# Optimization experiments

Hardware: AMD Instinct MI355X
Metric: run time of the kernel (lower is better)

The kernel has to match this reference:

```python
import jax, jax.numpy as jnp
import numpy as np

N_HEAD = 16
N_KV_HEAD = 4
HEAD_DIM = 64  # n_embd // n_head = 1024 // 16
N_EMBD = 1024


def _alibi_bias(T, n_head, head_dim):
    # slopes: start = 2**(-2**(-(log2(H)-3))); slope_i = start**(i+1)
    start = 2.0 ** (-2.0 ** (-(np.log2(n_head) - 3.0)))
    slopes = jnp.asarray(start ** np.arange(1, n_head + 1), dtype=jnp.float32)  # [H]
    rel = (jnp.arange(T, dtype=jnp.float32)[None, :]
           - jnp.arange(T, dtype=jnp.float32)[:, None])  # [T,T], rel[i,j] = j - i
    bias = slopes[:, None, None] * rel[None, :, :]  # [H,T,T]
    # Faithful to the torch module: masked_fill(-inf) is then OVERWRITTEN by
    # torch.tril, which zeroes the upper triangle. Net effect: lower-tri alibi
    # values, 0 above the diagonal (NO causal masking).
    bias = jnp.tril(bias)
    return bias * (head_dim ** -0.5)  # extra scale applied in forward


def setup_inputs() -> dict:
    key = jax.random.key(0)
    ks = jax.random.split(key, 5)
    B, T, C = 4, 2048, N_EMBD
    w_scale = 0.02
    return {
        "x": jax.random.normal(ks[0], (B, T, C), dtype=jnp.float32),
        "Wq": jax.random.normal(ks[1], (C, C), dtype=jnp.float32) * w_scale,
        "Wkv": jax.random.normal(ks[2], (2 * N_KV_HEAD * HEAD_DIM, C), dtype=jnp.float32) * w_scale,
        "Wproj": jax.random.normal(ks[3], (C, C), dtype=jnp.float32) * w_scale,
        "bproj": jnp.zeros((C,), dtype=jnp.float32),
    }


def reference(x, Wq, Wkv, Wproj, bproj):
    B, T, C = x.shape
    H, KVH, D = N_HEAD, N_KV_HEAD, HEAD_DIM
    ratio = H // KVH

    q = jnp.einsum('btc,ec->bte', x, Wq).reshape(B, T, H, D).transpose(0, 2, 1, 3)  # [B,H,T,D]
    kv = jnp.einsum('btc,ec->bte', x, Wkv)  # [B,T,2*KVH*D]
    k, v = jnp.split(kv, 2, axis=-1)
    k = k.reshape(B, T, KVH, D).transpose(0, 2, 1, 3)  # [B,KVH,T,D]
    v = v.reshape(B, T, KVH, D).transpose(0, 2, 1, 3)
    # torch .repeat tiles whole blocks: query head h uses kv head h % KVH
    k = jnp.tile(k, (1, ratio, 1, 1))  # [B,H,T,D]
    v = jnp.tile(v, (1, ratio, 1, 1))

    bias = _alibi_bias(T, H, D)  # [H,T,T], already *= D**-0.5
    scores = jnp.einsum('bhtd,bhsd->bhts', q, k) * (D ** -0.5) + bias[None]
    attn = jax.nn.softmax(scores, axis=-1)
    out = jnp.einsum('bhts,bhsd->bhtd', attn, v)  # [B,H,T,D]
    out = out.transpose(0, 2, 1, 3).reshape(B, T, C)
    return jnp.einsum('btc,ec->bte', out, Wproj) + bproj
```

## Files before the change

kernel.cpp:

```cpp
#include <hip/hip_runtime.h>
#include <hip/hip_bf16.h>
#include <cstdint>

typedef __bf16 bf16;
typedef bf16 bf16x4 __attribute__((ext_vector_type(4)));
typedef bf16 bf16x8 __attribute__((ext_vector_type(8)));
typedef float f32x4 __attribute__((ext_vector_type(4)));

#define MFMA16(a, b, c) __builtin_amdgcn_mfma_f32_16x16x32_bf16((a), (b), (c), 0, 0, 0)

__device__ inline void async16(const bf16* g, bf16* l) {
  __builtin_amdgcn_global_load_lds(
      (const __attribute__((address_space(1))) void*)g,
      (__attribute__((address_space(3))) void*)l, 16, 0, 0);
}

__device__ inline void lds_barrier() {
  asm volatile("s_waitcnt lgkmcnt(0)\n\ts_barrier" ::: "memory");
}

__global__ void cast_f32_to_bf16(const float* __restrict__ src,
                                 bf16* __restrict__ dst, int n4) {
  int i = blockIdx.x * blockDim.x + threadIdx.x;
  if (i < n4) {
    const float4 v = ((const float4*)src)[i];
    bf16x4 o;
    o.x = (bf16)v.x; o.y = (bf16)v.y; o.z = (bf16)v.z; o.w = (bf16)v.w;
    ((bf16x4*)dst)[i] = o;
  }
}

__global__ __launch_bounds__(256, 2)
void gemm_qkv(const bf16* __restrict__ A, const bf16* __restrict__ B,
              bf16* __restrict__ qb, bf16* __restrict__ kb, bf16* __restrict__ vb) {
  constexpr int K = 1024;
  __shared__ bf16 sA[128 * 64];
  __shared__ bf16 sB[128 * 64];
  const int tid = threadIdx.x;
  const int lane = tid & 63, wid = tid >> 6;
  const int col = lane & 15, quad = lane >> 4;
  const int wm = wid >> 1, wn = wid & 1;
  const int m0 = blockIdx.y * 128, n0 = blockIdx.x * 128;
  const int c7 = col & 7;

  f32x4 acc[4][4];
  const f32x4 z = {0.f, 0.f, 0.f, 0.f};
#pragma unroll
  for (int mi = 0; mi < 4; mi++)
#pragma unroll
    for (int ni = 0; ni < 4; ni++) acc[mi][ni] = z;

  for (int k0 = 0; k0 < K; k0 += 64) {
    __syncthreads();
#pragma unroll
    for (int c = 0; c < 4; ++c) {
      const int idx = c * 256 + tid;
      const int row = idx >> 3, kc = idx & 7;
      const int gkc = kc ^ (row & 7);
      async16(&A[(size_t)(m0 + row) * K + k0 + gkc * 8], &sA[idx * 8]);
      async16(&B[(size_t)(n0 + row) * K + k0 + gkc * 8], &sB[idx * 8]);
    }
    __syncthreads();
#pragma unroll
    for (int ks = 0; ks < 2; ++ks) {
      bf16x8 af[4], bfr[4];
#pragma unroll
      for (int i = 0; i < 4; i++)
        af[i] = *(const bf16x8*)&sA[(wm * 64 + i * 16 + col) * 64 +
                                    (((ks * 4 + quad) ^ c7) << 3)];
#pragma unroll
      for (int i = 0; i < 4; i++)
        bfr[i] = *(const bf16x8*)&sB[(wn * 64 + i * 16 + col) * 64 +
                                     (((ks * 4 + quad) ^ c7) << 3)];
#pragma unroll
      for (int mi = 0; mi < 4; mi++)
#pragma unroll
        for (int ni = 0; ni < 4; ni++)
          acc[mi][ni] = MFMA16(af[mi], bfr[ni], acc[mi][ni]);
    }
  }
#pragma unroll
  for (int mi = 0; mi < 4; mi++) {
#pragma unroll
    for (int ni = 0; ni < 4; ni++) {
      const int e = n0 + wn * 64 + ni * 16 + col;
#pragma unroll
      for (int r = 0; r < 4; r++) {
        const int m = m0 + wm * 64 + mi * 16 + quad * 4 + r;
        const int bb = m >> 11, t = m & 2047;
        const bf16 val = (bf16)acc[mi][ni][r];
        if (e < 1024) {
          qb[(((size_t)bb * 16 + (e >> 6)) * 2048 + t) * 64 + (e & 63)] = val;
        } else if (e < 1280) {
          const int f = e - 1024;
          kb[(((size_t)bb * 4 + (f >> 6)) * 2048 + t) * 64 + (f & 63)] = val;
        } else {
          const int f = e - 1280;
          vb[(((size_t)bb * 4 + (f >> 6)) * 2048 + t) * 64 + (f & 63)] = val;
        }
      }
    }
  }
}

__global__ __launch_bounds__(256, 2)
void gemm_proj(const bf16* __restrict__ A, const bf16* __restrict__ B,
               const float* __restrict__ bias, float* __restrict__ out) {
  constexpr int K = 1024;
  __shared__ bf16 sA[128 * 64];
  __shared__ bf16 sB[128 * 64];
  const int tid = threadIdx.x;
  const int lane = tid & 63, wid = tid >> 6;
  const int col = lane & 15, quad = lane >> 4;
  const int wm = wid >> 1, wn = wid & 1;
  const int m0 = blockIdx.y * 128, n0 = blockIdx.x * 128;
  const int c7 = col & 7;

  f32x4 acc[4][4];
  const f32x4 z = {0.f, 0.f, 0.f, 0.f};
#pragma unroll
  for (int mi = 0; mi < 4; mi++)
#pragma unroll
    for (int ni = 0; ni < 4; ni++) acc[mi][ni] = z;

  for (int k0 = 0; k0 < K; k0 += 64) {
    __syncthreads();
#pragma unroll
    for (int c = 0; c < 4; ++c) {
      const int idx = c * 256 + tid;
      const int row = idx >> 3, kc = idx & 7;
      const int gkc = kc ^ (row & 7);
      async16(&A[(size_t)(m0 + row) * K + k0 + gkc * 8], &sA[idx * 8]);
      async16(&B[(size_t)(n0 + row) * K + k0 + gkc * 8], &sB[idx * 8]);
    }
    __syncthreads();
#pragma unroll
    for (int ks = 0; ks < 2; ++ks) {
      bf16x8 af[4], bfr[4];
#pragma unroll
      for (int i = 0; i < 4; i++)
        af[i] = *(const bf16x8*)&sA[(wm * 64 + i * 16 + col) * 64 +
                                    (((ks * 4 + quad) ^ c7) << 3)];
#pragma unroll
      for (int i = 0; i < 4; i++)
        bfr[i] = *(const bf16x8*)&sB[(wn * 64 + i * 16 + col) * 64 +
                                     (((ks * 4 + quad) ^ c7) << 3)];
#pragma unroll
      for (int mi = 0; mi < 4; mi++)
#pragma unroll
        for (int ni = 0; ni < 4; ni++)
          acc[mi][ni] = MFMA16(af[mi], bfr[ni], acc[mi][ni]);
    }
  }
#pragma unroll
  for (int mi = 0; mi < 4; mi++) {
#pragma unroll
    for (int ni = 0; ni < 4; ni++) {
      const int e = n0 + wn * 64 + ni * 16 + col;
      const float be = bias[e];
#pragma unroll
      for (int r = 0; r < 4; r++) {
        const int m = m0 + wm * 64 + mi * 16 + quad * 4 + r;
        out[(size_t)m * 1024 + e] = acc[mi][ni][r] + be;
      }
    }
  }
}

__global__ __launch_bounds__(256, 2)
void attn_alibi(const bf16* __restrict__ qb, const bf16* __restrict__ kb,
                const bf16* __restrict__ vb, bf16* __restrict__ ob) {
  __shared__ bf16 sK[64 * 72];
  __shared__ bf16 sVt[64 * 72];
  __shared__ bf16 sPt[4][64 * 72];
  __shared__ float sL[4][64];
  const int tid = threadIdx.x;
  const int lane = tid & 63, wid = tid >> 6;
  const int col = lane & 15, quad = lane >> 4;
  const int bh = blockIdx.y;
  const int b = bh >> 4, h = bh & 15, kvh = h & 3;
  const int qbase = __builtin_amdgcn_readfirstlane(blockIdx.x * 256 + wid * 64);

  const bf16* qptr = qb + ((size_t)(b * 16 + h) * 2048 + qbase) * 64;
  const bf16* kptr = kb + ((size_t)(b * 4 + kvh) * 2048) * 64;
  const bf16* vptr = vb + ((size_t)(b * 4 + kvh) * 2048) * 64;

  bf16x8 bq[4][2];
#pragma unroll
  for (int ni = 0; ni < 4; ni++)
#pragma unroll
    for (int ks = 0; ks < 2; ks++)
      bq[ni][ks] = *(const bf16x8*)&qptr[(ni * 16 + col) * 64 + ks * 32 + quad * 8];

  f32x4 O[4][4];
  const f32x4 z = {0.f, 0.f, 0.f, 0.f};
#pragma unroll
  for (int mi = 0; mi < 4; mi++)
#pragma unroll
    for (int nd = 0; nd < 4; nd++) O[mi][nd] = z;
  float lsum[4] = {0.f, 0.f, 0.f, 0.f};

  const float c1 = 0.125f * 1.44269504f;
  const float cb = exp2f(-0.5f * (float)(h + 1)) * c1;
  const int qoff = quad * 4 - col;

  const int r0 = tid >> 3, r1 = 32 + (tid >> 3), kc = tid & 7;

  bf16x8 kr0, kr1, vr0, vr1;
  kr0 = *(const bf16x8*)&kptr[(size_t)r0 * 64 + kc * 8];
  kr1 = *(const bf16x8*)&kptr[(size_t)r1 * 64 + kc * 8];
  vr0 = *(const bf16x8*)&vptr[(size_t)r0 * 64 + kc * 8];
  vr1 = *(const bf16x8*)&vptr[(size_t)r1 * 64 + kc * 8];

  for (int c0 = 0; c0 < 2048; c0 += 64) {
    lds_barrier();
    *(bf16x8*)&sK[r0 * 72 + kc * 8] = kr0;
    *(bf16x8*)&sK[r1 * 72 + kc * 8] = kr1;
    {
      const int blk0 = r0 >> 3, rl0 = r0 & 7;
      const int blk1 = r1 >> 3, rl1 = r1 & 7;
#pragma unroll
      for (int j = 0; j < 8; j++) {
        sVt[(kc * 8 + j) * 72 + ((blk0 ^ kc) << 3) + rl0] = vr0[j];
        sVt[(kc * 8 + j) * 72 + ((blk1 ^ kc) << 3) + rl1] = vr1[j];
      }
    }
    {
      const int cn = (c0 + 64 < 2048) ? c0 + 64 : 0;
      kr0 = *(const bf16x8*)&kptr[(size_t)(cn + r0) * 64 + kc * 8];
      kr1 = *(const bf16x8*)&kptr[(size_t)(cn + r1) * 64 + kc * 8];
      vr0 = *(const bf16x8*)&vptr[(size_t)(cn + r0) * 64 + kc * 8];
      vr1 = *(const bf16x8*)&vptr[(size_t)(cn + r1) * 64 + kc * 8];
    }
    lds_barrier();

    f32x4 S[4][4];
#pragma unroll
    for (int mi = 0; mi < 4; mi++)
#pragma unroll
      for (int ni = 0; ni < 4; ni++) S[mi][ni] = z;
#pragma unroll
    for (int ks = 0; ks < 2; ks++) {
      bf16x8 ak[4];
#pragma unroll
      for (int mi = 0; mi < 4; mi++)
        ak[mi] = *(const bf16x8*)&sK[(mi * 16 + col) * 72 + ks * 32 + quad * 8];
#pragma unroll
      for (int mi = 0; mi < 4; mi++)
#pragma unroll
        for (int ni = 0; ni < 4; ni++)
          S[mi][ni] = MFMA16(ak[mi], bq[ni][ks], S[mi][ni]);
    }

    bf16* sp = sPt[wid];
#pragma unroll
    for (int ni = 0; ni < 4; ni++) {
      f32x4 p[4];
#pragma unroll
      for (int mi = 0; mi < 4; mi++) {
        const int U = c0 + mi * 16 - qbase - ni * 16;
        if (U <= -15) {
          const float bb = cb * (float)(U + qoff);
#pragma unroll
          for (int r = 0; r < 4; r++)
            p[mi][r] = __builtin_amdgcn_exp2f(S[mi][ni][r] * c1 + (bb + cb * (float)r));
        } else if (U >= 16) {
#pragma unroll
          for (int r = 0; r < 4; r++)
            p[mi][r] = __builtin_amdgcn_exp2f(S[mi][ni][r] * c1);
        } else {
          const float relf = (float)(U + qoff);
#pragma unroll
          for (int r = 0; r < 4; r++) {
            const float rr = relf + (float)r;
            const float bb = (rr <= 0.f) ? cb * rr : 0.f;
            p[mi][r] = __builtin_amdgcn_exp2f(S[mi][ni][r] * c1 + bb);
          }
        }
      }
      f32x4 t = (p[0] + p[1]) + (p[2] + p[3]);
      lsum[ni] += (t.x + t.y) + (t.z + t.w);
#pragma unroll
      for (int mi = 0; mi < 4; mi++) {
        bf16x4 w;
#pragma unroll
        for (int r = 0; r < 4; r++) w[r] = (bf16)p[mi][r];
        *(bf16x4*)&sp[(ni * 16 + col) * 72 + mi * 16 + quad * 4] = w;
      }
    }

#pragma unroll
    for (int ks = 0; ks < 2; ks++) {
      bf16x8 ap[4], bv[4];
#pragma unroll
      for (int mi = 0; mi < 4; mi++)
        ap[mi] = *(const bf16x8*)&sp[(mi * 16 + col) * 72 + ks * 32 + quad * 8];
#pragma unroll
      for (int nd = 0; nd < 4; nd++) {
        const int d = nd * 16 + col;
        bv[nd] = *(const bf16x8*)&sVt[d * 72 + (((ks * 4 + quad) ^ (d >> 3)) << 3)];
      }
#pragma unroll
      for (int mi = 0; mi < 4; mi++)
#pragma unroll
        for (int nd = 0; nd < 4; nd++)
          O[mi][nd] = MFMA16(ap[mi], bv[nd], O[mi][nd]);
    }
  }

#pragma unroll
  for (int ni = 0; ni < 4; ni++) {
    float l = lsum[ni];
    l += __shfl_xor(l, 16);
    l += __shfl_xor(l, 32);
    lsum[ni] = l;
  }
  __syncthreads();
  if (quad == 0) {
#pragma unroll
    for (int ni = 0; ni < 4; ni++) sL[wid][ni * 16 + col] = lsum[ni];
  }
  __syncthreads();

#pragma unroll
  for (int mi = 0; mi < 4; mi++) {
    const f32x4 lv = *(const f32x4*)&sL[wid][mi * 16 + quad * 4];
#pragma unroll
    for (int r = 0; r < 4; r++) {
      const float inv = 1.0f / lv[r];
      const int t = qbase + mi * 16 + quad * 4 + r;
#pragma unroll
      for (int nd = 0; nd < 4; nd++) {
        ob[((size_t)b * 2048 + t) * 1024 + h * 64 + nd * 16 + col] =
            (bf16)(O[mi][nd][r] * inv);
      }
    }
  }
}

extern "C" void kernel_launch(void* const* d_in, const int* in_sizes, int n_in,
                              void* d_out, int out_size, void* d_ws, size_t ws_size,
                              hipStream_t stream) {
  const float* x     = (const float*)d_in[0];
  const float* Wq    = (const float*)d_in[1];
  const float* Wkv   = (const float*)d_in[2];
  const float* Wproj = (const float*)d_in[3];
  const float* bproj = (const float*)d_in[4];
  float* out = (float*)d_out;

  bf16* xb  = (bf16*)d_ws;
  bf16* w1b = xb  + 8388608;
  bf16* wpb = w1b + 1572864;
  bf16* qb  = wpb + 1048576;
  bf16* kb  = qb  + 8388608;
  bf16* vb  = kb  + 2097152;
  bf16* aob = vb  + 2097152;

  cast_f32_to_bf16<<<8192, 256, 0, stream>>>(x, xb, 2097152);
  cast_f32_to_bf16<<<1024, 256, 0, stream>>>(Wq, w1b, 262144);
  cast_f32_to_bf16<<<512, 256, 0, stream>>>(Wkv, w1b + 1048576, 131072);
  cast_f32_to_bf16<<<1024, 256, 0, stream>>>(Wproj, wpb, 262144);

  gemm_qkv<<<dim3(12, 64), 256, 0, stream>>>(xb, w1b, qb, kb, vb);
  attn_alibi<<<dim3(8, 64), 256, 0, stream>>>(qb, kb, vb, aob);
  gemm_proj<<<dim3(8, 64), 256, 0, stream>>>(aob, wpb, bproj, out);
}
```

Baseline: 280.8 us.

## Fold softmax scale into Q, compute row sums via MFMA, swizzle LDS tiles

Q is pre-multiplied by the combined softmax and log2e scale in the QKV GEMM epilogue, which removes a multiply per score in attention. The softmax denominator is now accumulated by an extra MFMA against a vector of ones instead of per-lane FP32 adds plus shuffles and an LDS reduction. The K and P LDS tiles drop their padding in favour of XOR swizzling, and V transpose stores are paired into bf16x2 writes. This adds one MFMA per O block and rounds Q to bf16 after scaling, which slightly changes numerics.

```diff
diff --git a/kernel.cpp b/kernel.cpp
--- a/kernel.cpp
+++ b/kernel.cpp
@@ -3,20 +3,19 @@
 #include <cstdint>
 
 typedef __bf16 bf16;
+typedef bf16 bf16x2 __attribute__((ext_vector_type(2)));
 typedef bf16 bf16x4 __attribute__((ext_vector_type(4)));
 typedef bf16 bf16x8 __attribute__((ext_vector_type(8)));
 typedef float f32x4 __attribute__((ext_vector_type(4)));
 
 #define MFMA16(a, b, c) __builtin_amdgcn_mfma_f32_16x16x32_bf16((a), (b), (c), 0, 0, 0)
+
+#define QSCALE 0.18033688011112042f
 
 __device__ inline void async16(const bf16* g, bf16* l) {
   __builtin_amdgcn_global_load_lds(
       (const __attribute__((address_space(1))) void*)g,
       (__attribute__((address_space(3))) void*)l, 16, 0, 0);
-}
-
-__device__ inline void lds_barrier() {
-  asm volatile("s_waitcnt lgkmcnt(0)\n\ts_barrier" ::: "memory");
 }
 
 __global__ void cast_f32_to_bf16(const float* __restrict__ src,
@@ -88,15 +87,17 @@
       for (int r = 0; r < 4; r++) {
         const int m = m0 + wm * 64 + mi * 16 + quad * 4 + r;
         const int bb = m >> 11, t = m & 2047;
-        const bf16 val = (bf16)acc[mi][ni][r];
         if (e < 1024) {
-          qb[(((size_t)bb * 16 + (e >> 6)) * 2048 + t) * 64 + (e & 63)] = val;
+          qb[(((size_t)bb * 16 + (e >> 6)) * 2048 + t) * 64 + (e & 63)] =
+              (bf16)(acc[mi][ni][r] * QSCALE);
         } else if (e < 1280) {
           const int f = e - 1024;
-          kb[(((size_t)bb * 4 + (f >> 6)) * 2048 + t) * 64 + (f & 63)] = val;
+          kb[(((size_t)bb * 4 + (f >> 6)) * 2048 + t) * 64 + (f & 63)] =
+              (bf16)acc[mi][ni][r];
         } else {
           const int f = e - 1280;
-          vb[(((size_t)bb * 4 + (f >> 6)) * 2048 + t) * 64 + (f & 63)] = val;
+          vb[(((size_t)bb * 4 + (f >> 6)) * 2048 + t) * 64 + (f & 63)] =
+              (bf16)acc[mi][ni][r];
         }
       }
     }
@@ -170,13 +171,13 @@
 __global__ __launch_bounds__(256, 2)
 void attn_alibi(const bf16* __restrict__ qb, const bf16* __restrict__ kb,
                 const bf16* __restrict__ vb, bf16* __restrict__ ob) {
-  __shared__ bf16 sK[64 * 72];
+  __shared__ bf16 sK[64 * 64];
   __shared__ bf16 sVt[64 * 72];
-  __shared__ bf16 sPt[4][64 * 72];
-  __shared__ float sL[4][64];
+  __shared__ bf16 sPt[4][64 * 64];
   const int tid = threadIdx.x;
   const int lane = tid & 63, wid = tid >> 6;
   const int col = lane & 15, quad = lane >> 4;
+  const int c7 = col & 7;
   const int bh = blockIdx.y;
   const int b = bh >> 4, h = bh & 15, kvh = h & 3;
   const int qbase = __builtin_amdgcn_readfirstlane(blockIdx.x * 256 + wid * 64);
@@ -192,47 +193,53 @@
     for (int ks = 0; ks < 2; ks++)
       bq[ni][ks] = *(const bf16x8*)&qptr[(ni * 16 + col) * 64 + ks * 32 + quad * 8];
 
+  bf16x8 bones;
+#pragma unroll
+  for (int j = 0; j < 8; j++) bones[j] = (bf16)1.0f;
+
   f32x4 O[4][4];
+  f32x4 Osum[4];
   const f32x4 z = {0.f, 0.f, 0.f, 0.f};
 #pragma unroll
-  for (int mi = 0; mi < 4; mi++)
+  for (int mi = 0; mi < 4; mi++) {
+    Osum[mi] = z;
 #pragma unroll
     for (int nd = 0; nd < 4; nd++) O[mi][nd] = z;
-  float lsum[4] = {0.f, 0.f, 0.f, 0.f};
-
-  const float c1 = 0.125f * 1.44269504f;
-  const float cb = exp2f(-0.5f * (float)(h + 1)) * c1;
+  }
+
+  const float cb = exp2f(-0.5f * (float)(h + 1)) * QSCALE;
   const int qoff = quad * 4 - col;
 
-  const int r0 = tid >> 3, r1 = 32 + (tid >> 3), kc = tid & 7;
-
-  bf16x8 kr0, kr1, vr0, vr1;
-  kr0 = *(const bf16x8*)&kptr[(size_t)r0 * 64 + kc * 8];
-  kr1 = *(const bf16x8*)&kptr[(size_t)r1 * 64 + kc * 8];
-  vr0 = *(const bf16x8*)&vptr[(size_t)r0 * 64 + kc * 8];
-  vr1 = *(const bf16x8*)&vptr[(size_t)r1 * 64 + kc * 8];
+  const int rk0 = tid >> 3, rk1 = 32 + rk0, kc = tid & 7;
+  const int rv = rk0 * 2;
+  const int blkv = rv >> 3, rlv = rv & 7;
+  const int kx = (kc ^ (rk0 & 7)) << 3;
+
+  bf16x8 kr0 = *(const bf16x8*)&kptr[(size_t)rk0 * 64 + kc * 8];
+  bf16x8 kr1 = *(const bf16x8*)&kptr[(size_t)rk1 * 64 + kc * 8];
+  bf16x8 vr0 = *(const bf16x8*)&vptr[(size_t)rv * 64 + kc * 8];
+  bf16x8 vr1 = *(const bf16x8*)&vptr[(size_t)(rv + 1) * 64 + kc * 8];
 
   for (int c0 = 0; c0 < 2048; c0 += 64) {
-    lds_barrier();
-    *(bf16x8*)&sK[r0 * 72 + kc * 8] = kr0;
-    *(bf16x8*)&sK[r1 * 72 + kc * 8] = kr1;
-    {
-      const int blk0 = r0 >> 3, rl0 = r0 & 7;
-      const int blk1 = r1 >> 3, rl1 = r1 & 7;
-#pragma unroll
-      for (int j = 0; j < 8; j++) {
-        sVt[(kc * 8 + j) * 72 + ((blk0 ^ kc) << 3) + rl0] = vr0[j];
-        sVt[(kc * 8 + j) * 72 + ((blk1 ^ kc) << 3) + rl1] = vr1[j];
-      }
-    }
+    __syncthreads();
+    *(bf16x8*)&sK[rk0 * 64 + kx] = kr0;
+    *(bf16x8*)&sK[rk1 * 64 + kx] = kr1;
+#pragma unroll
+    for (int j = 0; j < 8; j++) {
+      bf16x2 pr;
+      pr.x = vr0[j];
+      pr.y = vr1[j];
+      *(bf16x2*)&sVt[(kc * 8 + j) * 72 + ((blkv ^ kc) << 3) + rlv] = pr;
+    }
+    __syncthreads();
+
     {
       const int cn = (c0 + 64 < 2048) ? c0 + 64 : 0;
-      kr0 = *(const bf16x8*)&kptr[(size_t)(cn + r0) * 64 + kc * 8];
-      kr1 = *(const bf16x8*)&kptr[(size_t)(cn + r1) * 64 + kc * 8];
-      vr0 = *(const bf16x8*)&vptr[(size_t)(cn + r0) * 64 + kc * 8];
-      vr1 = *(const bf16x8*)&vptr[(size_t)(cn + r1) * 64 + kc * 8];
-    }
-    lds_barrier();
+      kr0 = *(const bf16x8*)&kptr[(size_t)(cn + rk0) * 64 + kc * 8];
+      kr1 = *(const bf16x8*)&kptr[(size_t)(cn + rk1) * 64 + kc * 8];
+      vr0 = *(const bf16x8*)&vptr[(size_t)(cn + rv) * 64 + kc * 8];
+      vr1 = *(const bf16x8*)&vptr[(size_t)(cn + rv + 1) * 64 + kc * 8];
+    }
 
     f32x4 S[4][4];
 #pragma unroll
@@ -244,7 +251,8 @@
       bf16x8 ak[4];
 #pragma unroll
       for (int mi = 0; mi < 4; mi++)
-        ak[mi] = *(const bf16x8*)&sK[(mi * 16 + col) * 72 + ks * 32 + quad * 8];
+        ak[mi] = *(const bf16x8*)&sK[(mi * 16 + col) * 64 +
+                                     (((ks * 4 + quad) ^ c7) << 3)];
 #pragma unroll
       for (int mi = 0; mi < 4; mi++)
 #pragma unroll
@@ -255,37 +263,33 @@
     bf16* sp = sPt[wid];
 #pragma unroll
     for (int ni = 0; ni < 4; ni++) {
-      f32x4 p[4];
 #pragma unroll
       for (int mi = 0; mi < 4; mi++) {
         const int U = c0 + mi * 16 - qbase - ni * 16;
+        f32x4 p;
         if (U <= -15) {
           const float bb = cb * (float)(U + qoff);
 #pragma unroll
           for (int r = 0; r < 4; r++)
-            p[mi][r] = __builtin_amdgcn_exp2f(S[mi][ni][r] * c1 + (bb + cb * (float)r));
+            p[r] = __builtin_amdgcn_exp2f(S[mi][ni][r] + (bb + cb * (float)r));
         } else if (U >= 16) {
 #pragma unroll
           for (int r = 0; r < 4; r++)
-            p[mi][r] = __builtin_amdgcn_exp2f(S[mi][ni][r] * c1);
+            p[r] = __builtin_amdgcn_exp2f(S[mi][ni][r]);
         } else {
           const float relf = (float)(U + qoff);
 #pragma unroll
           for (int r = 0; r < 4; r++) {
             const float rr = relf + (float)r;
             const float bb = (rr <= 0.f) ? cb * rr : 0.f;
-            p[mi][r] = __builtin_amdgcn_exp2f(S[mi][ni][r] * c1 + bb);
+            p[r] = __builtin_amdgcn_exp2f(S[mi][ni][r] + bb);
           }
         }
-      }
-      f32x4 t = (p[0] + p[1]) + (p[2] + p[3]);
-      lsum[ni] += (t.x + t.y) + (t.z + t.w);
-#pragma unroll
-      for (int mi = 0; mi < 4; mi++) {
         bf16x4 w;
 #pragma unroll
-        for (int r = 0; r < 4; r++) w[r] = (bf16)p[mi][r];
-        *(bf16x4*)&sp[(ni * 16 + col) * 72 + mi * 16 + quad * 4] = w;
+        for (int r = 0; r < 4; r++) w[r] = (bf16)p[r];
+        *(bf16x4*)&sp[(ni * 16 + col) * 64 +
+                      (((2 * mi + (quad >> 1)) ^ c7) << 3) + ((quad & 1) << 2)] = w;
       }
     }
 
@@ -294,40 +298,28 @@
       bf16x8 ap[4], bv[4];
 #pragma unroll
       for (int mi = 0; mi < 4; mi++)
-        ap[mi] = *(const bf16x8*)&sp[(mi * 16 + col) * 72 + ks * 32 + quad * 8];
+        ap[mi] = *(const bf16x8*)&sp[(mi * 16 + col) * 64 +
+                                     (((ks * 4 + quad) ^ c7) << 3)];
 #pragma unroll
       for (int nd = 0; nd < 4; nd++) {
         const int d = nd * 16 + col;
         bv[nd] = *(const bf16x8*)&sVt[d * 72 + (((ks * 4 + quad) ^ (d >> 3)) << 3)];
       }
 #pragma unroll
-      for (int mi = 0; mi < 4; mi++)
+      for (int mi = 0; mi < 4; mi++) {
 #pragma unroll
         for (int nd = 0; nd < 4; nd++)
           O[mi][nd] = MFMA16(ap[mi], bv[nd], O[mi][nd]);
-    }
-  }
-
-#pragma unroll
-  for (int ni = 0; ni < 4; ni++) {
-    float l = lsum[ni];
-    l += __shfl_xor(l, 16);
-    l += __shfl_xor(l, 32);
-    lsum[ni] = l;
-  }
-  __syncthreads();
-  if (quad == 0) {
-#pragma unroll
-    for (int ni = 0; ni < 4; ni++) sL[wid][ni * 16 + col] = lsum[ni];
-  }
-  __syncthreads();
+        Osum[mi] = MFMA16(ap[mi], bones, Osum[mi]);
+      }
+    }
+  }
 
 #pragma unroll
   for (int mi = 0; mi < 4; mi++) {
-    const f32x4 lv = *(const f32x4*)&sL[wid][mi * 16 + quad * 4];
 #pragma unroll
     for (int r = 0; r < 4; r++) {
-      const float inv = 1.0f / lv[r];
+      const float inv = 1.0f / Osum[mi][r];
       const int t = qbase + mi * 16 + quad * 4 + r;
 #pragma unroll
       for (int nd = 0; nd < 4; nd++) {
```

After: 248.5 us. 11.5% less time.
